# Kernel optimization log

Hardware: AMD Instinct MI355X
Metric: run time of the kernel (lower is better)

Reference implementation:

```python
import jax, jax.numpy as jnp
import numpy as np

TAU = 0.8
N, D = 4096, 512

def _proj(x, W, b):
    # nn.Linear then ELU (torch Linear: x @ W.T + b)
    return jax.nn.elu(x @ W.T + b)

def setup_inputs() -> dict:
    key = jax.random.key(0)
    k1, k2, k3, k4, k5 = jax.random.split(key, 5)
    v1 = jax.random.normal(k1, (N, D), dtype=jnp.float32)
    v2 = jax.random.normal(k2, (N, D), dtype=jnp.float32)
    pos = jax.random.uniform(k3, (N, N), dtype=jnp.float32)
    neg = jax.random.uniform(k4, (N, N), dtype=jnp.float32)
    W = jax.random.normal(k5, (D, D), dtype=jnp.float32) * (1.414 / np.sqrt(D))
    b = jnp.zeros((D,), dtype=jnp.float32)
    return {"v1_embs": v1, "v2_embs": v2, "pos": pos, "neg": neg, "W_proj": W, "b_proj": b}

def reference(v1_embs, v2_embs, pos, neg, W_proj, b_proj):
    z1 = _proj(v1_embs, W_proj, b_proj)
    z2 = _proj(v2_embs, W_proj, b_proj)
    # cosine-similarity style: dot / (|z1||z2|) / tau, then exp
    n1 = jnp.linalg.norm(z1, axis=-1, keepdims=True)  # [N,1]
    n2 = jnp.linalg.norm(z2, axis=-1, keepdims=True)  # [N,1]
    dots = z1 @ z2.T                                   # [N,N]
    sim = jnp.exp(dots / (n1 * n2.T) / TAU)
    sim_pos = sim * pos
    sim_neg = sim * neg
    ratio = sim_pos.sum() / (sim_pos + sim_neg).sum()
    return -jnp.log(ratio)
```

## Files before the change

### kernel.cpp

```cpp
#include <hip/hip_runtime.h>
#include <hip/hip_bf16.h>
#include <math.h>

#define NROWS 4096
#define DDIM  512
#define INV_TAU 1.25f

typedef __attribute__((ext_vector_type(8))) short short8;
typedef __attribute__((ext_vector_type(4))) float f32x4;

__device__ inline void gload_lds16(const void* g, void* l) {
  __builtin_amdgcn_global_load_lds(
      (const __attribute__((address_space(1))) void*)g,
      (__attribute__((address_space(3))) void*)l, 16, 0, 0);
}

__device__ inline unsigned short f2bf(float f) {
  __hip_bfloat16 h = __float2bfloat16(f);
  return __builtin_bit_cast(unsigned short, h);
}
__device__ inline float bf2f(unsigned short u) {
  return __bfloat162float(__builtin_bit_cast(__hip_bfloat16, u));
}

__device__ inline unsigned f2e4m3(float s) {
  unsigned b = __builtin_bit_cast(unsigned, s);
  return (b + 0x80000u - 0x3C000000u) >> 20;
}
__device__ inline float e4m32f(unsigned u8) {
  return __builtin_bit_cast(float, (u8 << 20) + 0x3C000000u);
}

__global__ void convert_kernel(const float* __restrict__ v1,
                               const float* __restrict__ v2,
                               const float* __restrict__ W,
                               unsigned short* __restrict__ v1b,
                               unsigned short* __restrict__ v2b,
                               unsigned short* __restrict__ Wb,
                               float* __restrict__ nsq1,
                               float* __restrict__ nsq2) {
  int idx = blockIdx.x * blockDim.x + threadIdx.x;
  if (idx < NROWS) { nsq1[idx] = 0.f; nsq2[idx] = 0.f; }
  const int TOTV = (NROWS * DDIM) / 4;
  const int TOTW = (DDIM * DDIM) / 4;
  const int total = 2 * TOTV + TOTW;
  const int stride = gridDim.x * blockDim.x;
  for (int i = idx; i < total; i += stride) {
    const float4* src; unsigned short* dst; int j;
    if (i < TOTV)            { src = (const float4*)v1; dst = v1b; j = i; }
    else if (i < 2 * TOTV)   { src = (const float4*)v2; dst = v2b; j = i - TOTV; }
    else                     { src = (const float4*)W;  dst = Wb;  j = i - 2 * TOTV; }
    float4 x = src[j];
    ushort4 o;
    o.x = f2bf(x.x); o.y = f2bf(x.y); o.z = f2bf(x.z); o.w = f2bf(x.w);
    *(ushort4*)&dst[j * 4] = o;
  }
}

__global__ __launch_bounds__(256) void proj_kernel(
    const unsigned short* __restrict__ v1b, const unsigned short* __restrict__ v2b,
    const unsigned short* __restrict__ Wb,  const float* __restrict__ bias,
    unsigned short* __restrict__ z1b, unsigned short* __restrict__ z2b,
    float* __restrict__ nsq1, float* __restrict__ nsq2) {
  __shared__ __align__(16) unsigned short As[128 * 32];
  __shared__ __align__(16) unsigned short Bs[128 * 32];
  const int tid = threadIdx.x;
  const int wid = tid >> 6, lane = tid & 63;
  const int wm = wid >> 1, wn = wid & 1;
  const int l15 = lane & 15, l4 = lane >> 4;

  const int zsel = blockIdx.z;
  const unsigned short* Ag = (zsel ? v2b : v1b) + (size_t)blockIdx.y * 128 * DDIM;
  const unsigned short* Bg = Wb + (size_t)blockIdx.x * 128 * DDIM;
  unsigned short* Z = (zsel ? z2b : z1b);
  float* nsq = (zsel ? nsq2 : nsq1);

  f32x4 acc[4][4];
#pragma unroll
  for (int m = 0; m < 4; ++m)
#pragma unroll
    for (int n = 0; n < 4; ++n) acc[m][n] = (f32x4){0.f, 0.f, 0.f, 0.f};

  for (int kt = 0; kt < DDIM; kt += 32) {
#pragma unroll
    for (int i = 0; i < 2; ++i) {
      int off = i * 4096 + tid * 16;
      int row = off >> 6;
      int kb  = off & 63;
      gload_lds16((const char*)(Ag + row * DDIM + kt) + kb,
                  (char*)As + i * 4096 + wid * 1024);
      gload_lds16((const char*)(Bg + row * DDIM + kt) + kb,
                  (char*)Bs + i * 4096 + wid * 1024);
    }
    asm volatile("s_waitcnt vmcnt(0)" ::: "memory");
    __syncthreads();
    short8 av[4], bv[4];
#pragma unroll
    for (int m = 0; m < 4; ++m)
      av[m] = *(const short8*)&As[(wm * 64 + m * 16 + l15) * 32 + l4 * 8];
#pragma unroll
    for (int n = 0; n < 4; ++n)
      bv[n] = *(const short8*)&Bs[(wn * 64 + n * 16 + l15) * 32 + l4 * 8];
#pragma unroll
    for (int m = 0; m < 4; ++m)
#pragma unroll
      for (int n = 0; n < 4; ++n)
        acc[m][n] = __builtin_amdgcn_mfma_f32_16x16x32_bf16(
            av[m], bv[n], acc[m][n], 0, 0, 0);
    __syncthreads();
  }

  const int rowBase = blockIdx.y * 128 + wm * 64;
  const int colBase = blockIdx.x * 128 + wn * 64;
  float bcol[4];
#pragma unroll
  for (int n = 0; n < 4; ++n) bcol[n] = bias[colBase + n * 16 + l15];
#pragma unroll
  for (int m = 0; m < 4; ++m) {
#pragma unroll
    for (int reg = 0; reg < 4; ++reg) {
      int gRow = rowBase + m * 16 + l4 * 4 + reg;
      float rs = 0.f;
#pragma unroll
      for (int n = 0; n < 4; ++n) {
        int gCol = colBase + n * 16 + l15;
        float y = acc[m][n][reg] + bcol[n];
        float zv = (y > 0.f) ? y : expm1f(y);
        unsigned short zb = f2bf(zv);
        Z[(size_t)gRow * DDIM + gCol] = zb;
        float zf = bf2f(zb);
        rs += zf * zf;
      }
      rs += __shfl_xor(rs, 1, 64);
      rs += __shfl_xor(rs, 2, 64);
      rs += __shfl_xor(rs, 4, 64);
      rs += __shfl_xor(rs, 8, 64);
      if (l15 == 0) atomicAdd(&nsq[gRow], rs);
    }
  }
}

__global__ __launch_bounds__(256, 4) void dotsA_kernel(
    const unsigned short* __restrict__ z1b, const unsigned short* __restrict__ z2b,
    const float* __restrict__ nsq1, const float* __restrict__ nsq2,
    unsigned char* __restrict__ sim) {
  __shared__ __align__(16) char smem[2][16384];

  const int tid = threadIdx.x;
  const int wid = tid >> 6, lane = tid & 63;
  const int wm = wid >> 1, wn = wid & 1;
  const int l15 = lane & 15, l4 = lane >> 4;

  const int bid = blockIdx.x;
  const int by = bid >> 5, bx = bid & 31;

  const unsigned short* Ag = z1b + (size_t)by * 128 * DDIM;
  const unsigned short* Bg = z2b + (size_t)bx * 128 * DDIM;

  f32x4 acc[4][4];
#pragma unroll
  for (int m = 0; m < 4; ++m)
#pragma unroll
    for (int n = 0; n < 4; ++n) acc[m][n] = (f32x4){0.f, 0.f, 0.f, 0.f};

#define STAGE(buf, t)                                                          \
  {                                                                            \
    _Pragma("unroll")                                                          \
    for (int i = 0; i < 2; ++i) {                                              \
      int off = i * 4096 + tid * 16;                                           \
      int row = off >> 6;                                                      \
      int gsw = ((off >> 4) & 3) ^ ((row >> 1) & 3);                           \
      gload_lds16((const char*)Ag + row * 1024 + (t) * 64 + gsw * 16,          \
                  smem[buf] + i * 4096 + wid * 1024);                          \
      gload_lds16((const char*)Bg + row * 1024 + (t) * 64 + gsw * 16,          \
                  smem[buf] + 8192 + i * 4096 + wid * 1024);                   \
    }                                                                          \
  }

  STAGE(0, 0);
  STAGE(1, 1);

  const int aswz = (l4 ^ ((l15 >> 1) & 3)) * 8;

#pragma unroll
  for (int t = 0; t < 16; ++t) {
    if (t < 15) asm volatile("s_waitcnt vmcnt(4)" ::: "memory");
    else        asm volatile("s_waitcnt vmcnt(0)" ::: "memory");
    __builtin_amdgcn_s_barrier();
    const unsigned short* As = (const unsigned short*)smem[t & 1];
    const unsigned short* Bs = (const unsigned short*)(smem[t & 1] + 8192);
    short8 av[4], bv[4];
#pragma unroll
    for (int m = 0; m < 4; ++m)
      av[m] = *(const short8*)&As[(wm * 64 + m * 16 + l15) * 32 + aswz];
#pragma unroll
    for (int n = 0; n < 4; ++n)
      bv[n] = *(const short8*)&Bs[(wn * 64 + n * 16 + l15) * 32 + aswz];
#pragma unroll
    for (int m = 0; m < 4; ++m)
#pragma unroll
      for (int n = 0; n < 4; ++n)
        acc[m][n] = __builtin_amdgcn_mfma_f32_16x16x32_bf16(
            av[m], bv[n], acc[m][n], 0, 0, 0);
    __builtin_amdgcn_s_barrier();
    if (t < 14) STAGE(t & 1, t + 2);
  }
#undef STAGE

  const int rowBase = by * 128 + wm * 64;
  const int colBase = bx * 128 + wn * 64;

  float rs2[4], rs1[4][4];
#pragma unroll
  for (int n = 0; n < 4; ++n) rs2[n] = rsqrtf(nsq2[colBase + n * 16 + l15]);
#pragma unroll
  for (int m = 0; m < 4; ++m)
#pragma unroll
    for (int reg = 0; reg < 4; ++reg)
      rs1[m][reg] = rsqrtf(nsq1[rowBase + m * 16 + l4 * 4 + reg]);

  unsigned char* sB = (unsigned char*)smem;
#pragma unroll
  for (int m = 0; m < 4; ++m)
#pragma unroll
    for (int reg = 0; reg < 4; ++reg) {
      int lrow = wm * 64 + m * 16 + l4 * 4 + reg;
#pragma unroll
      for (int n = 0; n < 4; ++n) {
        float s = __expf(acc[m][n][reg] * (rs1[m][reg] * rs2[n]) * INV_TAU);
        sB[lrow * 128 + wn * 64 + n * 16 + l15] = (unsigned char)f2e4m3(s);
      }
    }
  __syncthreads();
  {
    int r = tid >> 1, h = tid & 1;
    const uint4* src = (const uint4*)(sB + r * 128 + h * 64);
    uint4 w0 = src[0], w1 = src[1], w2 = src[2], w3 = src[3];
    uint4* dst = (uint4*)(sim + (size_t)(by * 128 + r) * NROWS + bx * 128 + h * 64);
    dst[0] = w0; dst[1] = w1; dst[2] = w2; dst[3] = w3;
  }
}

__global__ __launch_bounds__(256) void reduce_kernel(
    const unsigned char* __restrict__ sim, const float* __restrict__ pos,
    const float* __restrict__ neg, double* __restrict__ partials) {
  const int tid = threadIdx.x;
  const int lane = tid & 63;
  const int wave = (blockIdx.x * 256 + tid) >> 6;
  const size_t base = (size_t)wave * 1024 + (size_t)lane * 4;

  f32x4 p[4], g[4]; unsigned s[4];
#pragma unroll
  for (int it = 0; it < 4; ++it) {
    size_t off = base + (size_t)it * 256;
    p[it] = __builtin_nontemporal_load((const f32x4*)(pos + off));
    g[it] = __builtin_nontemporal_load((const f32x4*)(neg + off));
    s[it] = *(const unsigned*)(sim + off);
  }

  float sumP = 0.f, sumG = 0.f;
#pragma unroll
  for (int it = 0; it < 4; ++it) {
    float s0 = e4m32f((s[it]      ) & 0x7Fu);
    float s1 = e4m32f((s[it] >>  8) & 0x7Fu);
    float s2 = e4m32f((s[it] >> 16) & 0x7Fu);
    float s3 = e4m32f((s[it] >> 24) & 0x7Fu);
    sumP += s0 * p[it][0] + s1 * p[it][1] + s2 * p[it][2] + s3 * p[it][3];
    sumG += s0 * g[it][0] + s1 * g[it][1] + s2 * g[it][2] + s3 * g[it][3];
  }

#pragma unroll
  for (int sft = 1; sft < 64; sft <<= 1) {
    sumP += __shfl_xor(sumP, sft, 64);
    sumG += __shfl_xor(sumG, sft, 64);
  }
  __shared__ float redP[4], redG[4];
  const int wid = tid >> 6;
  if (lane == 0) { redP[wid] = sumP; redG[wid] = sumG; }
  __syncthreads();
  if (tid == 0) {
    double tp = (double)redP[0] + redP[1] + redP[2] + redP[3];
    double tg = (double)redG[0] + redG[1] + redG[2] + redG[3];
    partials[2 * blockIdx.x]     = tp;
    partials[2 * blockIdx.x + 1] = tp + tg;
  }
}

__global__ void finalize_kernel(const double* __restrict__ partials, int n,
                                float* __restrict__ out) {
  __shared__ double sp[256], st[256];
  int t = threadIdx.x;
  double a = 0.0, b = 0.0;
  for (int i = t; i < n; i += 256) {
    a += partials[2 * i];
    b += partials[2 * i + 1];
  }
  sp[t] = a; st[t] = b;
  __syncthreads();
  for (int s = 128; s > 0; s >>= 1) {
    if (t < s) { sp[t] += sp[t + s]; st[t] += st[t + s]; }
    __syncthreads();
  }
  if (t == 0) out[0] = (float)(log(st[0]) - log(sp[0]));
}

extern "C" void kernel_launch(void* const* d_in, const int* in_sizes, int n_in,
                              void* d_out, int out_size, void* d_ws, size_t ws_size,
                              hipStream_t stream) {
  (void)in_sizes; (void)n_in; (void)out_size; (void)ws_size;
  const float* v1   = (const float*)d_in[0];
  const float* v2   = (const float*)d_in[1];
  const float* pos  = (const float*)d_in[2];
  const float* neg  = (const float*)d_in[3];
  const float* W    = (const float*)d_in[4];
  const float* bias = (const float*)d_in[5];

  char* ws = (char*)d_ws;
  unsigned short* z1b = (unsigned short*)(ws + 0);
  unsigned short* z2b = (unsigned short*)(ws + 4194304);
  float* nsq1         = (float*)(ws + 8388608);
  float* nsq2         = (float*)(ws + 8404992);
  double* partials    = (double*)(ws + 8421376);
  unsigned short* v1b = (unsigned short*)(ws + 8486912);
  unsigned short* v2b = (unsigned short*)(ws + 12681216);
  unsigned short* Wb  = (unsigned short*)(ws + 16875520);
  unsigned char*  sim = (unsigned char*)(ws + 17399808);
  float* out = (float*)d_out;

  hipLaunchKernelGGL(convert_kernel, dim3(1024), dim3(256), 0, stream,
                     v1, v2, W, v1b, v2b, Wb, nsq1, nsq2);
  hipLaunchKernelGGL(proj_kernel, dim3(DDIM / 128, NROWS / 128, 2), dim3(256), 0, stream,
                     v1b, v2b, Wb, bias, z1b, z2b, nsq1, nsq2);
  hipLaunchKernelGGL(dotsA_kernel, dim3(1024), dim3(256), 0, stream,
                     z1b, z2b, nsq1, nsq2, sim);
  hipLaunchKernelGGL(reduce_kernel, dim3(4096), dim3(256), 0, stream,
                     sim, pos, neg, partials);
  hipLaunchKernelGGL(finalize_kernel, dim3(1), dim3(256), 0, stream,
                     partials, 4096, out);
}
```

Before: 86.48 us.

## Fuse sim GEMM with pos/neg reduction and overlap streaming across two tiles

```diff
diff --git a/kernel.cpp b/kernel.cpp
--- a/kernel.cpp
+++ b/kernel.cpp
@@ -140,22 +140,46 @@
   }
 }
 
-__global__ __launch_bounds__(256, 4) void dotsA_kernel(
+__global__ __launch_bounds__(256, 3) void dots_kernel(
     const unsigned short* __restrict__ z1b, const unsigned short* __restrict__ z2b,
     const float* __restrict__ nsq1, const float* __restrict__ nsq2,
-    unsigned char* __restrict__ sim) {
+    const float* __restrict__ pos, const float* __restrict__ neg,
+    double* __restrict__ partials) {
   __shared__ __align__(16) char smem[2][16384];
+  __shared__ __align__(16) unsigned char sCh[16384];
+  __shared__ float redP[4], redG[4];
 
   const int tid = threadIdx.x;
   const int wid = tid >> 6, lane = tid & 63;
   const int wm = wid >> 1, wn = wid & 1;
   const int l15 = lane & 15, l4 = lane >> 4;
+  const int l31 = lane & 31, lh = lane >> 5;
 
   const int bid = blockIdx.x;
-  const int by = bid >> 5, bx = bid & 31;
-
-  const unsigned short* Ag = z1b + (size_t)by * 128 * DDIM;
-  const unsigned short* Bg = z2b + (size_t)bx * 128 * DDIM;
+  const int by = bid >> 4;
+  const int bxA = (bid & 15) * 2, bxB = bxA + 1;
+  const int blockRow = by * 128;
+
+  const unsigned short* Ag  = z1b + (size_t)by * 128 * DDIM;
+  const unsigned short* BgA = z2b + (size_t)bxA * 128 * DDIM;
+  const unsigned short* BgB = z2b + (size_t)bxB * 128 * DDIM;
+
+  float rs1v[4][4];
+#pragma unroll
+  for (int m = 0; m < 4; ++m)
+#pragma unroll
+    for (int reg = 0; reg < 4; ++reg)
+      rs1v[m][reg] = rsqrtf(nsq1[blockRow + wm * 64 + m * 16 + l4 * 4 + reg]);
+  float rs2A[4], rs2B[4];
+#pragma unroll
+  for (int n = 0; n < 4; ++n) {
+    rs2A[n] = rsqrtf(nsq2[bxA * 128 + wn * 64 + n * 16 + l15]);
+    rs2B[n] = rsqrtf(nsq2[bxB * 128 + wn * 64 + n * 16 + l15]);
+  }
+
+  const int srow0 = wid * 32 + lh;
+  const int scol  = l31 * 4;
+  const int aswz = (l4 ^ ((l15 >> 1) & 3)) * 8;
 
   f32x4 acc[4][4];
 #pragma unroll
@@ -163,7 +187,7 @@
 #pragma unroll
     for (int n = 0; n < 4; ++n) acc[m][n] = (f32x4){0.f, 0.f, 0.f, 0.f};
 
-#define STAGE(buf, t)                                                          \
+#define STAGE(Bg, buf, t)                                                      \
   {                                                                            \
     _Pragma("unroll")                                                          \
     for (int i = 0; i < 2; ++i) {                                              \
@@ -172,101 +196,138 @@
       int gsw = ((off >> 4) & 3) ^ ((row >> 1) & 3);                           \
       gload_lds16((const char*)Ag + row * 1024 + (t) * 64 + gsw * 16,          \
                   smem[buf] + i * 4096 + wid * 1024);                          \
-      gload_lds16((const char*)Bg + row * 1024 + (t) * 64 + gsw * 16,          \
+      gload_lds16((const char*)(Bg) + row * 1024 + (t) * 64 + gsw * 16,        \
                   smem[buf] + 8192 + i * 4096 + wid * 1024);                   \
     }                                                                          \
   }
 
-  STAGE(0, 0);
-  STAGE(1, 1);
-
-  const int aswz = (l4 ^ ((l15 >> 1) & 3)) * 8;
-
+#define FRAGS_MFMA(buf)                                                        \
+  {                                                                            \
+    const unsigned short* As = (const unsigned short*)smem[buf];               \
+    const unsigned short* Bs = (const unsigned short*)(smem[buf] + 8192);      \
+    short8 av[4], bv[4];                                                       \
+    _Pragma("unroll")                                                          \
+    for (int m = 0; m < 4; ++m)                                                \
+      av[m] = *(const short8*)&As[(wm * 64 + m * 16 + l15) * 32 + aswz];       \
+    _Pragma("unroll")                                                          \
+    for (int n = 0; n < 4; ++n)                                                \
+      bv[n] = *(const short8*)&Bs[(wn * 64 + n * 16 + l15) * 32 + aswz];       \
+    _Pragma("unroll")                                                          \
+    for (int m = 0; m < 4; ++m)                                                \
+      _Pragma("unroll")                                                        \
+      for (int n = 0; n < 4; ++n)                                              \
+        acc[m][n] = __builtin_amdgcn_mfma_f32_16x16x32_bf16(                   \
+            av[m], bv[n], acc[m][n], 0, 0, 0);                                 \
+  }
+
+#define CONVERT(rs2)                                                           \
+  {                                                                            \
+    _Pragma("unroll")                                                          \
+    for (int m = 0; m < 4; ++m)                                                \
+      _Pragma("unroll")                                                        \
+      for (int reg = 0; reg < 4; ++reg) {                                      \
+        int row = wm * 64 + m * 16 + l4 * 4 + reg;                             \
+        _Pragma("unroll")                                                      \
+        for (int n = 0; n < 4; ++n) {                                          \
+          float s = __expf(acc[m][n][reg] * (rs1v[m][reg] * (rs2)[n]) * INV_TAU);\
+          sCh[row * 128 + wn * 64 + n * 16 + l15] = (unsigned char)f2e4m3(s);  \
+        }                                                                      \
+        acc[m][0][reg] = 0.f;                        \
+      }                                                                        \
+  }
+
+#define SDECODE_FMA(sb, p, g)                                                  \
+  {                                                                            \
+    float s0 = e4m32f((sb) & 0x7Fu), s1 = e4m32f(((sb) >> 8) & 0x7Fu);         \
+    float s2 = e4m32f(((sb) >> 16) & 0x7Fu), s3 = e4m32f(((sb) >> 24) & 0x7Fu);\
+    sumP += s0 * (p)[0] + s1 * (p)[1] + s2 * (p)[2] + s3 * (p)[3];             \
+    sumG += s0 * (g)[0] + s1 * (g)[1] + s2 * (g)[2] + s3 * (g)[3];             \
+  }
+
+  STAGE(BgA, 0, 0);
+  STAGE(BgA, 1, 1);
 #pragma unroll
   for (int t = 0; t < 16; ++t) {
     if (t < 15) asm volatile("s_waitcnt vmcnt(4)" ::: "memory");
     else        asm volatile("s_waitcnt vmcnt(0)" ::: "memory");
     __builtin_amdgcn_s_barrier();
-    const unsigned short* As = (const unsigned short*)smem[t & 1];
-    const unsigned short* Bs = (const unsigned short*)(smem[t & 1] + 8192);
-    short8 av[4], bv[4];
-#pragma unroll
-    for (int m = 0; m < 4; ++m)
-      av[m] = *(const short8*)&As[(wm * 64 + m * 16 + l15) * 32 + aswz];
-#pragma unroll
-    for (int n = 0; n < 4; ++n)
-      bv[n] = *(const short8*)&Bs[(wn * 64 + n * 16 + l15) * 32 + aswz];
-#pragma unroll
-    for (int m = 0; m < 4; ++m)
-#pragma unroll
-      for (int n = 0; n < 4; ++n)
-        acc[m][n] = __builtin_amdgcn_mfma_f32_16x16x32_bf16(
-            av[m], bv[n], acc[m][n], 0, 0, 0);
+    FRAGS_MFMA(t & 1);
     __builtin_amdgcn_s_barrier();
-    if (t < 14) STAGE(t & 1, t + 2);
-  }
-#undef STAGE
-
-  const int rowBase = by * 128 + wm * 64;
-  const int colBase = bx * 128 + wn * 64;
-
-  float rs2[4], rs1[4][4];
-#pragma unroll
-  for (int n = 0; n < 4; ++n) rs2[n] = rsqrtf(nsq2[colBase + n * 16 + l15]);
+    if (t < 14) STAGE(BgA, t & 1, t + 2);
+  }
+
+  STAGE(BgB, 0, 0);
+  STAGE(BgB, 1, 1);
+  __builtin_amdgcn_sched_barrier(0);
+  CONVERT(rs2A);
 #pragma unroll
   for (int m = 0; m < 4; ++m)
 #pragma unroll
-    for (int reg = 0; reg < 4; ++reg)
-      rs1[m][reg] = rsqrtf(nsq1[rowBase + m * 16 + l4 * 4 + reg]);
-
-  unsigned char* sB = (unsigned char*)smem;
-#pragma unroll
-  for (int m = 0; m < 4; ++m)
-#pragma unroll
-    for (int reg = 0; reg < 4; ++reg) {
-      int lrow = wm * 64 + m * 16 + l4 * 4 + reg;
-#pragma unroll
-      for (int n = 0; n < 4; ++n) {
-        float s = __expf(acc[m][n][reg] * (rs1[m][reg] * rs2[n]) * INV_TAU);
-        sB[lrow * 128 + wn * 64 + n * 16 + l15] = (unsigned char)f2e4m3(s);
+    for (int n = 0; n < 4; ++n) acc[m][n] = (f32x4){0.f, 0.f, 0.f, 0.f};
+  asm volatile("s_waitcnt lgkmcnt(0)" ::: "memory");
+  __builtin_amdgcn_s_barrier();
+
+  const float* posA = pos + (size_t)(blockRow + srow0) * NROWS + bxA * 128 + scol;
+  const float* negA = neg + (size_t)(blockRow + srow0) * NROWS + bxA * 128 + scol;
+  f32x4 pv0, pv1, gv0, gv1;
+  float sumP = 0.f, sumG = 0.f;
+#pragma unroll
+  for (int t = 0; t < 16; ++t) {
+    if (t == 0)      asm volatile("s_waitcnt vmcnt(4)" ::: "memory");
+    else if (t < 15) asm volatile("s_waitcnt vmcnt(6)" ::: "memory");
+    else             asm volatile("s_waitcnt vmcnt(2)" ::: "memory");
+    __builtin_amdgcn_s_barrier();
+    unsigned sb = 0;
+    if (t >= 2) sb = *(const unsigned*)&sCh[(srow0 + (t - 2) * 2) * 128 + scol];
+    FRAGS_MFMA(t & 1);
+    if (t >= 2) {
+      if ((t & 1) == 0) { SDECODE_FMA(sb, pv0, gv0); }
+      else              { SDECODE_FMA(sb, pv1, gv1); }
+    }
+    __builtin_amdgcn_s_barrier();
+    if (t < 14) STAGE(BgB, t & 1, t + 2);
+    __builtin_amdgcn_sched_barrier(0);
+    {
+      const float* pp = posA + (size_t)(t * 2) * NROWS;
+      const float* gg = negA + (size_t)(t * 2) * NROWS;
+      if ((t & 1) == 0) { pv0 = *(const f32x4*)pp; gv0 = *(const f32x4*)gg; }
+      else              { pv1 = *(const f32x4*)pp; gv1 = *(const f32x4*)gg; }
+    }
+    __builtin_amdgcn_sched_barrier(0);
+  }
+  asm volatile("s_waitcnt vmcnt(0)" ::: "memory");
+  {
+    unsigned sb14 = *(const unsigned*)&sCh[(srow0 + 28) * 128 + scol];
+    SDECODE_FMA(sb14, pv0, gv0);
+    unsigned sb15 = *(const unsigned*)&sCh[(srow0 + 30) * 128 + scol];
+    SDECODE_FMA(sb15, pv1, gv1);
+  }
+
+  __builtin_amdgcn_s_barrier();
+  CONVERT(rs2B);
+  asm volatile("s_waitcnt lgkmcnt(0)" ::: "memory");
+  __builtin_amdgcn_s_barrier();
+
+  const float* posB = pos + (size_t)(blockRow + srow0) * NROWS + bxB * 128 + scol;
+  const float* negB = neg + (size_t)(blockRow + srow0) * NROWS + bxB * 128 + scol;
+  pv0 = *(const f32x4*)posB;                       gv0 = *(const f32x4*)negB;
+  pv1 = *(const f32x4*)(posB + 2 * NROWS);         gv1 = *(const f32x4*)(negB + 2 * NROWS);
+#pragma unroll
+  for (int c = 0; c < 16; ++c) {
+    unsigned sb = *(const unsigned*)&sCh[(srow0 + c * 2) * 128 + scol];
+    if ((c & 1) == 0) {
+      SDECODE_FMA(sb, pv0, gv0);
+      if (c + 2 < 16) {
+        pv0 = *(const f32x4*)(posB + (size_t)((c + 2) * 2) * NROWS);
+        gv0 = *(const f32x4*)(negB + (size_t)((c + 2) * 2) * NROWS);
+      }
+    } else {
+      SDECODE_FMA(sb, pv1, gv1);
+      if (c + 2 < 16) {
+        pv1 = *(const f32x4*)(posB + (size_t)((c + 2) * 2) * NROWS);
+        gv1 = *(const f32x4*)(negB + (size_t)((c + 2) * 2) * NROWS);
       }
     }
-  __syncthreads();
-  {
-    int r = tid >> 1, h = tid & 1;
-    const uint4* src = (const uint4*)(sB + r * 128 + h * 64);
-    uint4 w0 = src[0], w1 = src[1], w2 = src[2], w3 = src[3];
-    uint4* dst = (uint4*)(sim + (size_t)(by * 128 + r) * NROWS + bx * 128 + h * 64);
-    dst[0] = w0; dst[1] = w1; dst[2] = w2; dst[3] = w3;
-  }
-}
-
-__global__ __launch_bounds__(256) void reduce_kernel(
-    const unsigned char* __restrict__ sim, const float* __restrict__ pos,
-    const float* __restrict__ neg, double* __restrict__ partials) {
-  const int tid = threadIdx.x;
-  const int lane = tid & 63;
-  const int wave = (blockIdx.x * 256 + tid) >> 6;
-  const size_t base = (size_t)wave * 1024 + (size_t)lane * 4;
-
-  f32x4 p[4], g[4]; unsigned s[4];
-#pragma unroll
-  for (int it = 0; it < 4; ++it) {
-    size_t off = base + (size_t)it * 256;
-    p[it] = __builtin_nontemporal_load((const f32x4*)(pos + off));
-    g[it] = __builtin_nontemporal_load((const f32x4*)(neg + off));
-    s[it] = *(const unsigned*)(sim + off);
-  }
-
-  float sumP = 0.f, sumG = 0.f;
-#pragma unroll
-  for (int it = 0; it < 4; ++it) {
-    float s0 = e4m32f((s[it]      ) & 0x7Fu);
-    float s1 = e4m32f((s[it] >>  8) & 0x7Fu);
-    float s2 = e4m32f((s[it] >> 16) & 0x7Fu);
-    float s3 = e4m32f((s[it] >> 24) & 0x7Fu);
-    sumP += s0 * p[it][0] + s1 * p[it][1] + s2 * p[it][2] + s3 * p[it][3];
-    sumG += s0 * g[it][0] + s1 * g[it][1] + s2 * g[it][2] + s3 * g[it][3];
   }
 
 #pragma unroll
@@ -274,16 +335,18 @@
     sumP += __shfl_xor(sumP, sft, 64);
     sumG += __shfl_xor(sumG, sft, 64);
   }
-  __shared__ float redP[4], redG[4];
-  const int wid = tid >> 6;
   if (lane == 0) { redP[wid] = sumP; redG[wid] = sumG; }
   __syncthreads();
   if (tid == 0) {
     double tp = (double)redP[0] + redP[1] + redP[2] + redP[3];
     double tg = (double)redG[0] + redG[1] + redG[2] + redG[3];
-    partials[2 * blockIdx.x]     = tp;
-    partials[2 * blockIdx.x + 1] = tp + tg;
-  }
+    partials[2 * bid]     = tp;
+    partials[2 * bid + 1] = tp + tg;
+  }
+#undef STAGE
+#undef FRAGS_MFMA
+#undef CONVERT
+#undef SDECODE_FMA
 }
 
 __global__ void finalize_kernel(const double* __restrict__ partials, int n,
@@ -324,17 +387,14 @@
   unsigned short* v1b = (unsigned short*)(ws + 8486912);
   unsigned short* v2b = (unsigned short*)(ws + 12681216);
   unsigned short* Wb  = (unsigned short*)(ws + 16875520);
-  unsigned char*  sim = (unsigned char*)(ws + 17399808);
   float* out = (float*)d_out;
 
   hipLaunchKernelGGL(convert_kernel, dim3(1024), dim3(256), 0, stream,
                      v1, v2, W, v1b, v2b, Wb, nsq1, nsq2);
   hipLaunchKernelGGL(proj_kernel, dim3(DDIM / 128, NROWS / 128, 2), dim3(256), 0, stream,
                      v1b, v2b, Wb, bias, z1b, z2b, nsq1, nsq2);
-  hipLaunchKernelGGL(dotsA_kernel, dim3(1024), dim3(256), 0, stream,
-                     z1b, z2b, nsq1, nsq2, sim);
-  hipLaunchKernelGGL(reduce_kernel, dim3(4096), dim3(256), 0, stream,
-                     sim, pos, neg, partials);
+  hipLaunchKernelGGL(dots_kernel, dim3(512), dim3(256), 0, stream,
+                     z1b, z2b, nsq1, nsq2, pos, neg, partials);
   hipLaunchKernelGGL(finalize_kernel, dim3(1), dim3(256), 0, stream,
-                     partials, 4096, out);
-}
+                     partials, 512, out);
+}
```

After: 100.1 us. 1.16x slower.

## Software-pipeline similarity GEMM and pos/neg reduction across row quarters in merged launches

Applied to the files above, without the earlier changes.

```diff
diff --git a/kernel.cpp b/kernel.cpp
--- a/kernel.cpp
+++ b/kernel.cpp
@@ -140,149 +140,152 @@
   }
 }
 
-__global__ __launch_bounds__(256, 4) void dotsA_kernel(
+__global__ __launch_bounds__(256, 4) void step_kernel(
     const unsigned short* __restrict__ z1b, const unsigned short* __restrict__ z2b,
     const float* __restrict__ nsq1, const float* __restrict__ nsq2,
-    unsigned char* __restrict__ sim) {
+    const float* __restrict__ pos, const float* __restrict__ neg,
+    unsigned char* __restrict__ sim, double* __restrict__ partials,
+    int qG, int qR, int pbase) {
   __shared__ __align__(16) char smem[2][16384];
-
   const int tid = threadIdx.x;
-  const int wid = tid >> 6, lane = tid & 63;
-  const int wm = wid >> 1, wn = wid & 1;
-  const int l15 = lane & 15, l4 = lane >> 4;
-
-  const int bid = blockIdx.x;
-  const int by = bid >> 5, bx = bid & 31;
-
-  const unsigned short* Ag = z1b + (size_t)by * 128 * DDIM;
-  const unsigned short* Bg = z2b + (size_t)bx * 128 * DDIM;
-
-  f32x4 acc[4][4];
-#pragma unroll
-  for (int m = 0; m < 4; ++m)
-#pragma unroll
-    for (int n = 0; n < 4; ++n) acc[m][n] = (f32x4){0.f, 0.f, 0.f, 0.f};
+
+  if (blockIdx.x < 256) {
+    if (qG < 0) return;
+    const int b = blockIdx.x;
+    const int by = qG * 8 + (b >> 5), bx = b & 31;
+
+    const int wid = tid >> 6, lane = tid & 63;
+    const int wm = wid >> 1, wn = wid & 1;
+    const int l15 = lane & 15, l4 = lane >> 4;
+
+    const unsigned short* Ag = z1b + (size_t)by * 128 * DDIM;
+    const unsigned short* Bg = z2b + (size_t)bx * 128 * DDIM;
+
+    f32x4 acc[4][4];
+#pragma unroll
+    for (int m = 0; m < 4; ++m)
+#pragma unroll
+      for (int n = 0; n < 4; ++n) acc[m][n] = (f32x4){0.f, 0.f, 0.f, 0.f};
 
 #define STAGE(buf, t)                                                          \
-  {                                                                            \
-    _Pragma("unroll")                                                          \
-    for (int i = 0; i < 2; ++i) {                                              \
-      int off = i * 4096 + tid * 16;                                           \
-      int row = off >> 6;                                                      \
-      int gsw = ((off >> 4) & 3) ^ ((row >> 1) & 3);                           \
-      gload_lds16((const char*)Ag + row * 1024 + (t) * 64 + gsw * 16,          \
-                  smem[buf] + i * 4096 + wid * 1024);                          \
-      gload_lds16((const char*)Bg + row * 1024 + (t) * 64 + gsw * 16,          \
-                  smem[buf] + 8192 + i * 4096 + wid * 1024);                   \
-    }                                                                          \
-  }
-
-  STAGE(0, 0);
-  STAGE(1, 1);
-
-  const int aswz = (l4 ^ ((l15 >> 1) & 3)) * 8;
-
-#pragma unroll
-  for (int t = 0; t < 16; ++t) {
-    if (t < 15) asm volatile("s_waitcnt vmcnt(4)" ::: "memory");
-    else        asm volatile("s_waitcnt vmcnt(0)" ::: "memory");
-    __builtin_amdgcn_s_barrier();
-    const unsigned short* As = (const unsigned short*)smem[t & 1];
-    const unsigned short* Bs = (const unsigned short*)(smem[t & 1] + 8192);
-    short8 av[4], bv[4];
-#pragma unroll
-    for (int m = 0; m < 4; ++m)
-      av[m] = *(const short8*)&As[(wm * 64 + m * 16 + l15) * 32 + aswz];
-#pragma unroll
-    for (int n = 0; n < 4; ++n)
-      bv[n] = *(const short8*)&Bs[(wn * 64 + n * 16 + l15) * 32 + aswz];
-#pragma unroll
-    for (int m = 0; m < 4; ++m)
+    {                                                                          \
+      _Pragma("unroll")                                                        \
+      for (int i = 0; i < 2; ++i) {                                            \
+        int off = i * 4096 + tid * 16;                                         \
+        int row = off >> 6;                                                    \
+        int gsw = ((off >> 4) & 3) ^ ((row >> 1) & 3);                         \
+        gload_lds16((const char*)Ag + row * 1024 + (t) * 64 + gsw * 16,        \
+                    smem[buf] + i * 4096 + wid * 1024);                        \
+        gload_lds16((const char*)Bg + row * 1024 + (t) * 64 + gsw * 16,        \
+                    smem[buf] + 8192 + i * 4096 + wid * 1024);                 \
+      }                                                                        \
+    }
+
+    STAGE(0, 0);
+    STAGE(1, 1);
+    const int aswz = (l4 ^ ((l15 >> 1) & 3)) * 8;
+
+#pragma unroll
+    for (int t = 0; t < 16; ++t) {
+      if (t < 15) asm volatile("s_waitcnt vmcnt(4)" ::: "memory");
+      else        asm volatile("s_waitcnt vmcnt(0)" ::: "memory");
+      __builtin_amdgcn_s_barrier();
+      const unsigned short* As = (const unsigned short*)smem[t & 1];
+      const unsigned short* Bs = (const unsigned short*)(smem[t & 1] + 8192);
+      short8 av[4], bv[4];
+#pragma unroll
+      for (int m = 0; m < 4; ++m)
+        av[m] = *(const short8*)&As[(wm * 64 + m * 16 + l15) * 32 + aswz];
 #pragma unroll
       for (int n = 0; n < 4; ++n)
-        acc[m][n] = __builtin_amdgcn_mfma_f32_16x16x32_bf16(
-            av[m], bv[n], acc[m][n], 0, 0, 0);
-    __builtin_amdgcn_s_barrier();
-    if (t < 14) STAGE(t & 1, t + 2);
-  }
+        bv[n] = *(const short8*)&Bs[(wn * 64 + n * 16 + l15) * 32 + aswz];
+#pragma unroll
+      for (int m = 0; m < 4; ++m)
+#pragma unroll
+        for (int n = 0; n < 4; ++n)
+          acc[m][n] = __builtin_amdgcn_mfma_f32_16x16x32_bf16(
+              av[m], bv[n], acc[m][n], 0, 0, 0);
+      __builtin_amdgcn_s_barrier();
+      if (t < 14) STAGE(t & 1, t + 2);
+    }
 #undef STAGE
 
-  const int rowBase = by * 128 + wm * 64;
-  const int colBase = bx * 128 + wn * 64;
-
-  float rs2[4], rs1[4][4];
-#pragma unroll
-  for (int n = 0; n < 4; ++n) rs2[n] = rsqrtf(nsq2[colBase + n * 16 + l15]);
-#pragma unroll
-  for (int m = 0; m < 4; ++m)
-#pragma unroll
-    for (int reg = 0; reg < 4; ++reg)
-      rs1[m][reg] = rsqrtf(nsq1[rowBase + m * 16 + l4 * 4 + reg]);
-
-  unsigned char* sB = (unsigned char*)smem;
-#pragma unroll
-  for (int m = 0; m < 4; ++m)
-#pragma unroll
-    for (int reg = 0; reg < 4; ++reg) {
-      int lrow = wm * 64 + m * 16 + l4 * 4 + reg;
-#pragma unroll
-      for (int n = 0; n < 4; ++n) {
-        float s = __expf(acc[m][n][reg] * (rs1[m][reg] * rs2[n]) * INV_TAU);
-        sB[lrow * 128 + wn * 64 + n * 16 + l15] = (unsigned char)f2e4m3(s);
+    const int rowBase = by * 128 + wm * 64;
+    const int colBase = bx * 128 + wn * 64;
+
+    float rs2[4], rs1[4][4];
+#pragma unroll
+    for (int n = 0; n < 4; ++n) rs2[n] = rsqrtf(nsq2[colBase + n * 16 + l15]);
+#pragma unroll
+    for (int m = 0; m < 4; ++m)
+#pragma unroll
+      for (int reg = 0; reg < 4; ++reg)
+        rs1[m][reg] = rsqrtf(nsq1[rowBase + m * 16 + l4 * 4 + reg]);
+
+    unsigned char* sB = (unsigned char*)smem;
+#pragma unroll
+    for (int m = 0; m < 4; ++m)
+#pragma unroll
+      for (int reg = 0; reg < 4; ++reg) {
+        int lrow = wm * 64 + m * 16 + l4 * 4 + reg;
+#pragma unroll
+        for (int n = 0; n < 4; ++n) {
+          float s = __expf(acc[m][n][reg] * (rs1[m][reg] * rs2[n]) * INV_TAU);
+          sB[lrow * 128 + wn * 64 + n * 16 + l15] = (unsigned char)f2e4m3(s);
+        }
       }
-    }
-  __syncthreads();
-  {
-    int r = tid >> 1, h = tid & 1;
-    const uint4* src = (const uint4*)(sB + r * 128 + h * 64);
-    uint4 w0 = src[0], w1 = src[1], w2 = src[2], w3 = src[3];
-    uint4* dst = (uint4*)(sim + (size_t)(by * 128 + r) * NROWS + bx * 128 + h * 64);
-    dst[0] = w0; dst[1] = w1; dst[2] = w2; dst[3] = w3;
-  }
-}
-
-__global__ __launch_bounds__(256) void reduce_kernel(
-    const unsigned char* __restrict__ sim, const float* __restrict__ pos,
-    const float* __restrict__ neg, double* __restrict__ partials) {
-  const int tid = threadIdx.x;
-  const int lane = tid & 63;
-  const int wave = (blockIdx.x * 256 + tid) >> 6;
-  const size_t base = (size_t)wave * 1024 + (size_t)lane * 4;
-
-  f32x4 p[4], g[4]; unsigned s[4];
-#pragma unroll
-  for (int it = 0; it < 4; ++it) {
-    size_t off = base + (size_t)it * 256;
-    p[it] = __builtin_nontemporal_load((const f32x4*)(pos + off));
-    g[it] = __builtin_nontemporal_load((const f32x4*)(neg + off));
-    s[it] = *(const unsigned*)(sim + off);
-  }
-
-  float sumP = 0.f, sumG = 0.f;
-#pragma unroll
-  for (int it = 0; it < 4; ++it) {
-    float s0 = e4m32f((s[it]      ) & 0x7Fu);
-    float s1 = e4m32f((s[it] >>  8) & 0x7Fu);
-    float s2 = e4m32f((s[it] >> 16) & 0x7Fu);
-    float s3 = e4m32f((s[it] >> 24) & 0x7Fu);
-    sumP += s0 * p[it][0] + s1 * p[it][1] + s2 * p[it][2] + s3 * p[it][3];
-    sumG += s0 * g[it][0] + s1 * g[it][1] + s2 * g[it][2] + s3 * g[it][3];
-  }
-
-#pragma unroll
-  for (int sft = 1; sft < 64; sft <<= 1) {
-    sumP += __shfl_xor(sumP, sft, 64);
-    sumG += __shfl_xor(sumG, sft, 64);
-  }
-  __shared__ float redP[4], redG[4];
-  const int wid = tid >> 6;
-  if (lane == 0) { redP[wid] = sumP; redG[wid] = sumG; }
-  __syncthreads();
-  if (tid == 0) {
-    double tp = (double)redP[0] + redP[1] + redP[2] + redP[3];
-    double tg = (double)redG[0] + redG[1] + redG[2] + redG[3];
-    partials[2 * blockIdx.x]     = tp;
-    partials[2 * blockIdx.x + 1] = tp + tg;
+    __syncthreads();
+    {
+      int r = tid >> 1, h = tid & 1;
+      const uint4* src = (const uint4*)(sB + r * 128 + h * 64);
+      uint4 w0 = src[0], w1 = src[1], w2 = src[2], w3 = src[3];
+      uint4* dst = (uint4*)(sim + (size_t)(by * 128 + r) * NROWS + bx * 128 + h * 64);
+      dst[0] = w0; dst[1] = w1; dst[2] = w2; dst[3] = w3;
+    }
+  } else {
+    if (qR < 0) return;
+    const int rb = blockIdx.x - 256;
+    const int lane = tid & 63;
+    const int wv = (rb * 256 + tid) >> 6;
+    const size_t base = (size_t)qR * 4194304 + (size_t)wv * 4096 + (size_t)lane * 4;
+
+    float sumP = 0.f, sumG = 0.f;
+#pragma unroll
+    for (int g = 0; g < 4; ++g) {
+      f32x4 p[4], q[4]; unsigned s[4];
+#pragma unroll
+      for (int it = 0; it < 4; ++it) {
+        size_t off = base + (size_t)(g * 4 + it) * 256;
+        p[it] = __builtin_nontemporal_load((const f32x4*)(pos + off));
+        q[it] = __builtin_nontemporal_load((const f32x4*)(neg + off));
+        s[it] = *(const unsigned*)(sim + off);
+      }
+#pragma unroll
+      for (int it = 0; it < 4; ++it) {
+        float s0 = e4m32f((s[it]      ) & 0x7Fu);
+        float s1 = e4m32f((s[it] >>  8) & 0x7Fu);
+        float s2 = e4m32f((s[it] >> 16) & 0x7Fu);
+        float s3 = e4m32f((s[it] >> 24) & 0x7Fu);
+        sumP += s0 * p[it][0] + s1 * p[it][1] + s2 * p[it][2] + s3 * p[it][3];
+        sumG += s0 * q[it][0] + s1 * q[it][1] + s2 * q[it][2] + s3 * q[it][3];
+      }
+    }
+
+#pragma unroll
+    for (int sft = 1; sft < 64; sft <<= 1) {
+      sumP += __shfl_xor(sumP, sft, 64);
+      sumG += __shfl_xor(sumG, sft, 64);
+    }
+    float* red = (float*)smem;
+    const int wid = tid >> 6;
+    if (lane == 0) { red[wid] = sumP; red[4 + wid] = sumG; }
+    __syncthreads();
+    if (tid == 0) {
+      double tp = (double)red[0] + red[1] + red[2] + red[3];
+      double tg = (double)red[4] + red[5] + red[6] + red[7];
+      partials[2 * (pbase + rb)]     = tp;
+      partials[2 * (pbase + rb) + 1] = tp + tg;
+    }
   }
 }
 
@@ -331,10 +334,16 @@
                      v1, v2, W, v1b, v2b, Wb, nsq1, nsq2);
   hipLaunchKernelGGL(proj_kernel, dim3(DDIM / 128, NROWS / 128, 2), dim3(256), 0, stream,
                      v1b, v2b, Wb, bias, z1b, z2b, nsq1, nsq2);
-  hipLaunchKernelGGL(dotsA_kernel, dim3(1024), dim3(256), 0, stream,
-                     z1b, z2b, nsq1, nsq2, sim);
-  hipLaunchKernelGGL(reduce_kernel, dim3(4096), dim3(256), 0, stream,
-                     sim, pos, neg, partials);
+  hipLaunchKernelGGL(step_kernel, dim3(512), dim3(256), 0, stream,
+                     z1b, z2b, nsq1, nsq2, pos, neg, sim, partials, 0, -1, 0);
+  hipLaunchKernelGGL(step_kernel, dim3(512), dim3(256), 0, stream,
+                     z1b, z2b, nsq1, nsq2, pos, neg, sim, partials, 1, 0, 0);
+  hipLaunchKernelGGL(step_kernel, dim3(512), dim3(256), 0, stream,
+                     z1b, z2b, nsq1, nsq2, pos, neg, sim, partials, 2, 1, 256);
+  hipLaunchKernelGGL(step_kernel, dim3(512), dim3(256), 0, stream,
+                     z1b, z2b, nsq1, nsq2, pos, neg, sim, partials, 3, 2, 512);
+  hipLaunchKernelGGL(step_kernel, dim3(512), dim3(256), 0, stream,
+                     z1b, z2b, nsq1, nsq2, pos, neg, sim, partials, -1, 3, 768);
   hipLaunchKernelGGL(finalize_kernel, dim3(1), dim3(256), 0, stream,
-                     partials, 4096, out);
-}
+                     partials, 1024, out);
+}
```

Measured after the change: 99.44 us. +15.0%, slower.
